# Kernel tuning notes

Hardware: AMD Instinct MI355X
Metric: run time of the kernel (lower is better)

## Reference

```python
import jax, jax.numpy as jnp
import numpy as np

N, F_IN, H1, H2, E = 100000, 256, 128, 64, 1600000


def _glorot(key, shape):
    lim = np.sqrt(6.0 / (shape[0] + shape[1]))
    return jax.random.uniform(key, shape, jnp.float32, -lim, lim)


def setup_inputs() -> dict:
    key = jax.random.key(0)
    ks = jax.random.split(key, 8)
    x = jax.random.normal(ks[0], (N, F_IN), jnp.float32)
    edge_index = jax.random.randint(ks[1], (2, E), 0, N, jnp.int64)
    return {
        "x": x,
        "w1": _glorot(ks[2], (F_IN, H1)),
        "b1": jnp.zeros((H1,), jnp.float32),
        "w2": _glorot(ks[3], (H1, H2)),
        "b2": jnp.zeros((H2,), jnp.float32),
        "w3": _glorot(ks[4], (H1, H2)),
        "b3": jnp.zeros((H2,), jnp.float32),
        "edge_index": edge_index,
    }


def _gcn_conv(x, w, b, src, dst, dinv_sqrt):
    # GCNConv: transform first, then symmetric-normalized aggregation with self-loops.
    h = x @ w                                   # [N, out]
    coef = dinv_sqrt[src] * dinv_sqrt[dst]      # [E]
    agg = jnp.zeros_like(h).at[dst].add(h[src] * coef[:, None])
    # self-loop contribution: coefficient deg^-1 per node
    agg = agg + h * (dinv_sqrt * dinv_sqrt)[:, None]
    return agg + b


def reference(x, w1, b1, w2, b2, w3, b3, edge_index):
    src, dst = edge_index[0], edge_index[1]
    n = x.shape[0]
    # degree including self-loop (edge weights all 1)
    deg = jnp.ones((n,), x.dtype).at[dst].add(1.0)
    dinv_sqrt = jax.lax.rsqrt(deg)
    hidden = jax.nn.relu(_gcn_conv(x, w1, b1, src, dst, dinv_sqrt))
    mu = _gcn_conv(hidden, w2, b2, src, dst, dinv_sqrt)
    logvar = _gcn_conv(hidden, w3, b3, src, dst, dinv_sqrt)
    return (mu, logvar)
```

## Files before the change

### kernel.cpp

```cpp
#include <hip/hip_runtime.h>


#define TPB 256
#define GSHIFT 9
#define GSIZE 512
#define PART_M 4096
#define GCAP 12288

typedef __attribute__((ext_vector_type(8))) short short8;
typedef __attribute__((ext_vector_type(4))) short short4v;
typedef __attribute__((ext_vector_type(4))) float floatx4;
typedef __attribute__((ext_vector_type(4))) unsigned int uint4v;

__device__ __forceinline__ void split2(float v, short& hi, short& lo) {
    unsigned u = __float_as_uint(v);
    float hf = __uint_as_float(u & 0xFFFF0000u);
    float lf = v - hf;
    hi = (short)(u >> 16);
    lo = (short)(__float_as_uint(lf) >> 16);
}

__device__ __forceinline__ short bf16_rtn(float v) {
    unsigned u = __float_as_uint(v);
    u += 0x7FFF + ((u >> 16) & 1);
    return (short)(u >> 16);
}

__device__ __forceinline__ void addrow(float* a, uint4v v) {
    a[0] += __uint_as_float(v[0] << 16); a[1] += __uint_as_float(v[0] & 0xFFFF0000u);
    a[2] += __uint_as_float(v[1] << 16); a[3] += __uint_as_float(v[1] & 0xFFFF0000u);
    a[4] += __uint_as_float(v[2] << 16); a[5] += __uint_as_float(v[2] & 0xFFFF0000u);
    a[6] += __uint_as_float(v[3] << 16); a[7] += __uint_as_float(v[3] & 0xFFFF0000u);
}

__device__ __forceinline__ void gather_accum(float* acc, const int* __restrict__ csr,
                                             int start, int deg, const uint4v* hp,
                                             int l16) {
    for (int jj = 0; jj < deg; jj += 16) {
        int rem = deg - jj;
        if (rem > 16) rem = 16;
        int il = (l16 < rem) ? l16 : rem - 1;
        int myIdx = csr[start + jj + il];
        int r = 0;
        for (; r + 3 < rem; r += 4) {
            int i0 = __shfl(myIdx, r + 0, 16);
            int i1 = __shfl(myIdx, r + 1, 16);
            int i2 = __shfl(myIdx, r + 2, 16);
            int i3 = __shfl(myIdx, r + 3, 16);
            uint4v v0 = hp[(size_t)i0 * 16 + l16];
            uint4v v1 = hp[(size_t)i1 * 16 + l16];
            uint4v v2 = hp[(size_t)i2 * 16 + l16];
            uint4v v3 = hp[(size_t)i3 * 16 + l16];
            addrow(acc, v0);
            addrow(acc, v1);
            addrow(acc, v2);
            addrow(acc, v3);
        }
        for (; r < rem; ++r) {
            int i = __shfl(myIdx, r, 16);
            addrow(acc, hp[(size_t)i * 16 + l16]);
        }
    }
}

__device__ __forceinline__ void gload_lds16(const void* g, void* l) {
    __builtin_amdgcn_global_load_lds(
        (const __attribute__((address_space(1))) unsigned int*)g,
        (__attribute__((address_space(3))) unsigned int*)l, 16, 0, 0);
}

__global__ __launch_bounds__(TPB) void prep_all(const float* __restrict__ w1,
                                                const float* __restrict__ w2,
                                                const float* __restrict__ b2,
                                                const float* __restrict__ w3,
                                                const float* __restrict__ b3,
                                                short* __restrict__ w1t_h,
                                                short* __restrict__ w1t_l,
                                                short* __restrict__ wct_h,
                                                short* __restrict__ wct_l,
                                                float* __restrict__ bcat,
                                                int* __restrict__ gcur) {
    int b = blockIdx.x, t0 = threadIdx.x;
    if (b < 128) {
        int t = b * TPB + t0;
        int k = t & 255, n = t >> 8;
        float v = w1[(size_t)k * 128 + n];
        short h, l;
        split2(v, h, l);
        w1t_h[t] = h;
        w1t_l[t] = l;
    } else if (b < 192) {
        int t = (b - 128) * TPB + t0;
        int k = t & 127, n = t >> 7;
        float v = (n < 64) ? w2[(size_t)k * 64 + n] : w3[(size_t)k * 64 + (n - 64)];
        short h, l;
        split2(v, h, l);
        wct_h[t] = h;
        wct_l[t] = l;
        if (t < 64) { bcat[t] = b2[t]; bcat[64 + t] = b3[t]; }
    } else {
        gcur[t0] = 0;
    }
}

__global__ __launch_bounds__(256) void partition_kernel(const int* __restrict__ src,
                                                        const int* __restrict__ dst,
                                                        int* __restrict__ gcur,
                                                        int* __restrict__ staged, int E) {
    __shared__ int sc[256];
    __shared__ int cur[256];
    __shared__ int gb[256];
    int t = threadIdx.x;
    int base = blockIdx.x * PART_M;
    int mloc = min(PART_M, E - base);
    int m4 = mloc >> 2;

    sc[t] = 0;
    cur[t] = 0;
    __syncthreads();
    const int4* d4 = (const int4*)(dst + base);
    const int4* s4 = (const int4*)(src + base);
    for (int k = t; k < m4; k += 256) {
        int4 v = d4[k];
        atomicAdd(&sc[v.x >> GSHIFT], 1);
        atomicAdd(&sc[v.y >> GSHIFT], 1);
        atomicAdd(&sc[v.z >> GSHIFT], 1);
        atomicAdd(&sc[v.w >> GSHIFT], 1);
    }
    for (int k = (m4 << 2) + t; k < mloc; k += 256)
        atomicAdd(&sc[dst[base + k] >> GSHIFT], 1);
    __syncthreads();
    int v = sc[t];
    gb[t] = v ? t * GCAP + atomicAdd(&gcur[t], v) : 0;
    __syncthreads();
    for (int k = t; k < m4; k += 256) {
        int4 dv = d4[k];
        int4 sv = s4[k];
        int b0 = dv.x >> GSHIFT;
        staged[gb[b0] + atomicAdd(&cur[b0], 1)] = (sv.x << GSHIFT) | (dv.x & (GSIZE - 1));
        int b1 = dv.y >> GSHIFT;
        staged[gb[b1] + atomicAdd(&cur[b1], 1)] = (sv.y << GSHIFT) | (dv.y & (GSIZE - 1));
        int b2 = dv.z >> GSHIFT;
        staged[gb[b2] + atomicAdd(&cur[b2], 1)] = (sv.z << GSHIFT) | (dv.z & (GSIZE - 1));
        int b3 = dv.w >> GSHIFT;
        staged[gb[b3] + atomicAdd(&cur[b3], 1)] = (sv.w << GSHIFT) | (dv.w & (GSIZE - 1));
    }
    for (int k = (m4 << 2) + t; k < mloc; k += 256) {
        int d = dst[base + k];
        int s = src[base + k];
        int b = d >> GSHIFT;
        staged[gb[b] + atomicAdd(&cur[b], 1)] = (s << GSHIFT) | (d & (GSIZE - 1));
    }
}

__global__ __launch_bounds__(512) void build_csr(const int* __restrict__ staged,
                                                 const int* __restrict__ gcur,
                                                 int* __restrict__ cnt,
                                                 float* __restrict__ dinv,
                                                 int* __restrict__ rowptr,
                                                 int* __restrict__ csr, int N) {
    __shared__ int pre[256];
    __shared__ int hist[512];
    __shared__ int sc[512];
    __shared__ int lrow[512];
    __shared__ int cur[512];
    int t = threadIdx.x;
    int g = blockIdx.x;
    int ngrp = (N + GSIZE - 1) >> GSHIFT;
    if (t < 256) pre[t] = (t < ngrp) ? gcur[t] : 0;
    hist[t] = 0;
    cur[t] = 0;
    __syncthreads();
#pragma unroll
    for (int off = 1; off < 256; off <<= 1) {
        int x = (t < 256 && t >= off) ? pre[t - off] : 0;
        __syncthreads();
        if (t < 256) pre[t] += x;
        __syncthreads();
    }
    int count = gcur[g];
    int s0_out = pre[g] - count;
    int s0_in = g * GCAP;
    for (int k = t; k < count; k += 512)
        atomicAdd(&hist[staged[s0_in + k] & (GSIZE - 1)], 1);
    __syncthreads();
    int v = hist[t];
    sc[t] = v;
    __syncthreads();
#pragma unroll
    for (int off = 1; off < 512; off <<= 1) {
        int x = (t >= off) ? sc[t - off] : 0;
        __syncthreads();
        sc[t] += x;
        __syncthreads();
    }
    int rp = s0_out + sc[t] - v;
    lrow[t] = rp;
    int node = (g << GSHIFT) + t;
    if (node < N) {
        rowptr[node] = rp;
        cnt[node] = v;
        dinv[node] = rsqrtf(1.0f + (float)v);
    }
    __syncthreads();
    for (int k = t; k < count; k += 512) {
        int p = staged[s0_in + k];
        int dl = p & (GSIZE - 1);
        int pos = lrow[dl] + atomicAdd(&cur[dl], 1);
        csr[pos] = p >> GSHIFT;
    }
}

__global__ __launch_bounds__(TPB) void gemm_mfma_f32in(const float* __restrict__ A,
                                                       const short* __restrict__ Bth,
                                                       const short* __restrict__ Btl,
                                                       const float* __restrict__ rs,
                                                       short* __restrict__ Cb, int M, int K) {
    __shared__ float Af[2][128 * 32];
    __shared__ short Bh[2][128 * 32];
    __shared__ short Bl[2][128 * 32];
    int t = threadIdx.x;
    int wave = t >> 6, lane = t & 63, quad = lane >> 4, l16 = lane & 15;
    int bm0 = blockIdx.x * 128;

    floatx4 acc[2][8];
#pragma unroll
    for (int mt = 0; mt < 2; ++mt)
#pragma unroll
        for (int nt = 0; nt < 8; ++nt) acc[mt][nt] = (floatx4){0.f, 0.f, 0.f, 0.f};

    auto stage = [&](int pb, int k0) {
#pragma unroll
        for (int i = 0; i < 4; ++i) {
            int g = i * 256 + t;
            int row = g >> 3, col = g & 7;
            int gr = bm0 + row;
            if (gr >= M) gr = M - 1;
            int scol = col ^ (row & 7);
            gload_lds16(A + (size_t)gr * K + k0 + scol * 4,
                        &Af[pb][(i * 256 + wave * 64) * 4]);
        }
#pragma unroll
        for (int i = 0; i < 2; ++i) {
            int g = i * 256 + t;
            int row = g >> 2, col = g & 3;
            int scol = col ^ ((row >> 1) & 3);
            size_t off = (size_t)row * K + k0 + scol * 8;
            int lb = (i * 256 + wave * 64) * 8;
            gload_lds16(Bth + off, &Bh[pb][lb]);
            gload_lds16(Btl + off, &Bl[pb][lb]);
        }
    };

    int nk = K >> 5;
    stage(0, 0);
    __syncthreads();
    int r0 = wave * 32 + l16;
    int ac0 = ((quad * 2 + 0) ^ (r0 & 7)) * 4;
    int ac1 = ((quad * 2 + 1) ^ (r0 & 7)) * 4;
    int bc = (quad ^ ((l16 >> 1) & 3)) * 8;
    for (int ks = 0; ks < nk; ++ks) {
        int pb = ks & 1;
        if (ks + 1 < nk) stage(pb ^ 1, (ks + 1) << 5);
        short8 a_h[2], a_l[2];
#pragma unroll
        for (int mt = 0; mt < 2; ++mt) {
            int r = r0 + mt * 16;
            float4 fa0 = *(const float4*)&Af[pb][r * 32 + ac0];
            float4 fa1 = *(const float4*)&Af[pb][r * 32 + ac1];
            short h, l;
            split2(fa0.x, h, l); a_h[mt][0] = h; a_l[mt][0] = l;
            split2(fa0.y, h, l); a_h[mt][1] = h; a_l[mt][1] = l;
            split2(fa0.z, h, l); a_h[mt][2] = h; a_l[mt][2] = l;
            split2(fa0.w, h, l); a_h[mt][3] = h; a_l[mt][3] = l;
            split2(fa1.x, h, l); a_h[mt][4] = h; a_l[mt][4] = l;
            split2(fa1.y, h, l); a_h[mt][5] = h; a_l[mt][5] = l;
            split2(fa1.z, h, l); a_h[mt][6] = h; a_l[mt][6] = l;
            split2(fa1.w, h, l); a_h[mt][7] = h; a_l[mt][7] = l;
        }
#pragma unroll
        for (int nt = 0; nt < 8; ++nt) {
            int bn = nt * 16 + l16;
            short8 b_h = *(const short8*)&Bh[pb][bn * 32 + bc];
            short8 b_l = *(const short8*)&Bl[pb][bn * 32 + bc];
#pragma unroll
            for (int mt = 0; mt < 2; ++mt) {
                acc[mt][nt] = __builtin_amdgcn_mfma_f32_16x16x32_bf16(a_l[mt], b_h, acc[mt][nt], 0, 0, 0);
                acc[mt][nt] = __builtin_amdgcn_mfma_f32_16x16x32_bf16(a_h[mt], b_l, acc[mt][nt], 0, 0, 0);
                acc[mt][nt] = __builtin_amdgcn_mfma_f32_16x16x32_bf16(a_h[mt], b_h, acc[mt][nt], 0, 0, 0);
            }
        }
        __syncthreads();
    }
#pragma unroll
    for (int mt = 0; mt < 2; ++mt)
#pragma unroll
        for (int reg = 0; reg < 4; ++reg) {
            int gr = bm0 + wave * 32 + mt * 16 + quad * 4 + reg;
            if (gr < M) {
                float s = rs[gr];
                short* cp = Cb + (size_t)gr * 128;
#pragma unroll
                for (int nt = 0; nt < 8; ++nt) cp[nt * 16 + l16] = bf16_rtn(acc[mt][nt][reg] * s);
            }
        }
}

__global__ __launch_bounds__(TPB) void gemm_mfma_bfin(const short* __restrict__ AH,
                                                      const short* __restrict__ AL,
                                                      const short* __restrict__ Bth,
                                                      const short* __restrict__ Btl,
                                                      const float* __restrict__ rs,
                                                      short* __restrict__ Cb, int M, int K) {
    __shared__ short Ah[2][128 * 32], Al[2][128 * 32];
    __shared__ short Bh[2][128 * 32], Bl[2][128 * 32];
    int t = threadIdx.x;
    int wave = t >> 6, lane = t & 63, quad = lane >> 4, l16 = lane & 15;
    int bm0 = blockIdx.x * 128;

    floatx4 acc[2][8];
#pragma unroll
    for (int mt = 0; mt < 2; ++mt)
#pragma unroll
        for (int nt = 0; nt < 8; ++nt) acc[mt][nt] = (floatx4){0.f, 0.f, 0.f, 0.f};

    auto stage = [&](int pb, int k0) {
#pragma unroll
        for (int i = 0; i < 2; ++i) {
            int g = i * 256 + t;
            int row = g >> 2, col = g & 3;
            int gr = bm0 + row;
            if (gr >= M) gr = M - 1;
            int scol = col ^ ((row >> 1) & 3);
            size_t off = (size_t)gr * K + k0 + scol * 8;
            int lb = (i * 256 + wave * 64) * 8;
            gload_lds16(AH + off, &Ah[pb][lb]);
            gload_lds16(AL + off, &Al[pb][lb]);
        }
#pragma unroll
        for (int i = 0; i < 2; ++i) {
            int g = i * 256 + t;
            int row = g >> 2, col = g & 3;
            int scol = col ^ ((row >> 1) & 3);
            size_t off = (size_t)row * K + k0 + scol * 8;
            int lb = (i * 256 + wave * 64) * 8;
            gload_lds16(Bth + off, &Bh[pb][lb]);
            gload_lds16(Btl + off, &Bl[pb][lb]);
        }
    };

    int nk = K >> 5;
    stage(0, 0);
    __syncthreads();
    int r0 = wave * 32 + l16;
    int ac = (quad ^ ((r0 >> 1) & 3)) * 8;
    int bc = (quad ^ ((l16 >> 1) & 3)) * 8;
    for (int ks = 0; ks < nk; ++ks) {
        int pb = ks & 1;
        if (ks + 1 < nk) stage(pb ^ 1, (ks + 1) << 5);
        short8 a_h[2], a_l[2];
#pragma unroll
        for (int mt = 0; mt < 2; ++mt) {
            int r = r0 + mt * 16;
            a_h[mt] = *(const short8*)&Ah[pb][r * 32 + ac];
            a_l[mt] = *(const short8*)&Al[pb][r * 32 + ac];
        }
#pragma unroll
        for (int nt = 0; nt < 8; ++nt) {
            int bn = nt * 16 + l16;
            short8 b_h = *(const short8*)&Bh[pb][bn * 32 + bc];
            short8 b_l = *(const short8*)&Bl[pb][bn * 32 + bc];
#pragma unroll
            for (int mt = 0; mt < 2; ++mt) {
                acc[mt][nt] = __builtin_amdgcn_mfma_f32_16x16x32_bf16(a_l[mt], b_h, acc[mt][nt], 0, 0, 0);
                acc[mt][nt] = __builtin_amdgcn_mfma_f32_16x16x32_bf16(a_h[mt], b_l, acc[mt][nt], 0, 0, 0);
                acc[mt][nt] = __builtin_amdgcn_mfma_f32_16x16x32_bf16(a_h[mt], b_h, acc[mt][nt], 0, 0, 0);
            }
        }
        __syncthreads();
    }
#pragma unroll
    for (int mt = 0; mt < 2; ++mt)
#pragma unroll
        for (int reg = 0; reg < 4; ++reg) {
            int gr = bm0 + wave * 32 + mt * 16 + quad * 4 + reg;
            if (gr < M) {
                float s = rs[gr];
                short* cp = Cb + (size_t)gr * 128;
#pragma unroll
                for (int nt = 0; nt < 8; ++nt) cp[nt * 16 + l16] = bf16_rtn(acc[mt][nt][reg] * s);
            }
        }
}

__global__ __launch_bounds__(TPB) void gather_hidden(const int* __restrict__ csr,
                                                     const int* __restrict__ rowptr,
                                                     const int* __restrict__ cnt,
                                                     const float* __restrict__ dinv,
                                                     const short* __restrict__ hs,
                                                     const float* __restrict__ b1,
                                                     short* __restrict__ hidH,
                                                     short* __restrict__ hidL, int N) {
    size_t t = (size_t)blockIdx.x * TPB + threadIdx.x;
    int nid = (int)(t >> 4);
    int lane = threadIdx.x & 15;
    if (nid >= N) return;
    int start = rowptr[nid];
    int deg = cnt[nid];
    const uint4v* hp = (const uint4v*)hs;
    float acc[8] = {0, 0, 0, 0, 0, 0, 0, 0};
    addrow(acc, hp[(size_t)nid * 16 + lane]);
    gather_accum(acc, csr, start, deg, hp, lane);
    float di = dinv[nid];
    float4 b0 = ((const float4*)b1)[lane * 2];
    float4 b1v = ((const float4*)b1)[lane * 2 + 1];
    float bb[8] = {b0.x, b0.y, b0.z, b0.w, b1v.x, b1v.y, b1v.z, b1v.w};
    unsigned hiw[8];
    short low[8];
#pragma unroll
    for (int i = 0; i < 8; ++i) {
        float h = fmaxf(fmaf(di, acc[i], bb[i]), 0.f);
        unsigned u = __float_as_uint(h);
        hiw[i] = u >> 16;
        float hf = __uint_as_float(u & 0xFFFF0000u);
        low[i] = bf16_rtn(h - hf);
    }
    uint4v ph, pl;
    ph[0] = hiw[0] | (hiw[1] << 16);
    ph[1] = hiw[2] | (hiw[3] << 16);
    ph[2] = hiw[4] | (hiw[5] << 16);
    ph[3] = hiw[6] | (hiw[7] << 16);
    pl[0] = (unsigned short)low[0] | ((unsigned)(unsigned short)low[1] << 16);
    pl[1] = (unsigned short)low[2] | ((unsigned)(unsigned short)low[3] << 16);
    pl[2] = (unsigned short)low[4] | ((unsigned)(unsigned short)low[5] << 16);
    pl[3] = (unsigned short)low[6] | ((unsigned)(unsigned short)low[7] << 16);
    ((uint4v*)hidH)[(size_t)nid * 16 + lane] = ph;
    ((uint4v*)hidL)[(size_t)nid * 16 + lane] = pl;
}

__global__ __launch_bounds__(TPB) void gather_out(const int* __restrict__ csr,
                                                  const int* __restrict__ rowptr,
                                                  const int* __restrict__ cnt,
                                                  const float* __restrict__ dinv,
                                                  const short* __restrict__ hs,
                                                  const float* __restrict__ bcat,
                                                  float* __restrict__ out, int N) {
    size_t t = (size_t)blockIdx.x * TPB + threadIdx.x;
    int nid = (int)(t >> 4);
    int lane = threadIdx.x & 15;
    if (nid >= N) return;
    int start = rowptr[nid];
    int deg = cnt[nid];
    const uint4v* hp = (const uint4v*)hs;
    float acc[8] = {0, 0, 0, 0, 0, 0, 0, 0};
    addrow(acc, hp[(size_t)nid * 16 + lane]);
    gather_accum(acc, csr, start, deg, hp, lane);
    float di = dinv[nid];
    float4 b0 = ((const float4*)bcat)[lane * 2];
    float4 b1v = ((const float4*)bcat)[lane * 2 + 1];
    floatx4 r0, r1;
    r0[0] = fmaf(di, acc[0], b0.x);
    r0[1] = fmaf(di, acc[1], b0.y);
    r0[2] = fmaf(di, acc[2], b0.z);
    r0[3] = fmaf(di, acc[3], b0.w);
    r1[0] = fmaf(di, acc[4], b1v.x);
    r1[1] = fmaf(di, acc[5], b1v.y);
    r1[2] = fmaf(di, acc[6], b1v.z);
    r1[3] = fmaf(di, acc[7], b1v.w);
    int f = lane * 8;
    float* dp = (f < 64) ? (out + (size_t)nid * 64 + f)
                         : (out + (size_t)N * 64 + (size_t)nid * 64 + (f - 64));
    __builtin_nontemporal_store(r0, (floatx4*)dp);
    __builtin_nontemporal_store(r1, (floatx4*)(dp + 4));
}

extern "C" void kernel_launch(void* const* d_in, const int* in_sizes, int n_in,
                              void* d_out, int out_size, void* d_ws, size_t ws_size,
                              hipStream_t stream) {
    const float* x  = (const float*)d_in[0];
    const float* w1 = (const float*)d_in[1];
    const float* b1 = (const float*)d_in[2];
    const float* w2 = (const float*)d_in[3];
    const float* b2 = (const float*)d_in[4];
    const float* w3 = (const float*)d_in[5];
    const float* b3 = (const float*)d_in[6];
    const int*   ei = (const int*)d_in[7];

    const int N = in_sizes[0] / 256;
    const int E = in_sizes[7] / 2;
    const int K1 = 256;

    float* out = (float*)d_out;

    size_t nh = (size_t)N * 128;
    short* hs1    = (short*)d_ws;
    short* hidH   = hs1 + nh;
    short* hidL   = hidH + nh;
    short* hs2    = hidL + nh;
    int*   cnt    = (int*)(hs2 + nh);
    float* dinv   = (float*)(cnt + N);
    int*   rowptr = (int*)(dinv + N);
    int*   cursor = rowptr + N;
    int*   bsum   = cursor + N;
    float* bcat   = (float*)(bsum + 512);
    short* w1t_h  = (short*)(bcat + 128);
    short* w1t_l  = w1t_h + 128 * 256;
    short* wct_h  = w1t_l + 128 * 256;
    short* wct_l  = wct_h + 128 * 128;
    int*   csr    = (int*)(wct_l + 128 * 128);

    const int* srcp = ei;
    const int* dstp = ei + E;

    const int ngrp = (N + GSIZE - 1) >> GSHIFT;
    int* gcur   = cursor;
    int* staged = (int*)hs2;

    prep_all<<<193, TPB, 0, stream>>>(w1, w2, b2, w3, b3, w1t_h, w1t_l, wct_h, wct_l,
                                      bcat, gcur);

    partition_kernel<<<(E + PART_M - 1) / PART_M, 256, 0, stream>>>(srcp, dstp, gcur,
                                                                    staged, E);
    build_csr<<<ngrp, 512, 0, stream>>>(staged, gcur, cnt, dinv, rowptr, csr, N);

    gemm_mfma_f32in<<<(N + 127) / 128, TPB, 0, stream>>>(x, w1t_h, w1t_l, dinv, hs1, N, K1);

    size_t gthreads = (size_t)N * 16;
    gather_hidden<<<(unsigned)((gthreads + TPB - 1) / TPB), TPB, 0, stream>>>(
        csr, rowptr, cnt, dinv, hs1, b1, hidH, hidL, N);

    gemm_mfma_bfin<<<(N + 127) / 128, TPB, 0, stream>>>(hidH, hidL, wct_h, wct_l, dinv, hs2, N, 128);

    gather_out<<<(unsigned)((gthreads + TPB - 1) / TPB), TPB, 0, stream>>>(
        csr, rowptr, cnt, dinv, hs2, bcat, out, N);
}
```

Baseline: 380.7 us.

## Fuse prep with partition and CSR build with first GEMM

Merges weight prep and edge partitioning into one launch, and runs the CSR build blocks and the first GEMM tiles in a single grid. The first GEMM no longer depends on dinv, so the source-side normalization moves into gather_hidden, which loads dinv per neighbor and applies it with an FMA. This removes two kernel launches and lets the CSR construction overlap the x@W1 GEMM. In exchange, gather_hidden does an extra dinv load and shuffle per edge, and gcur is now zeroed with a memset.

Result: no change. 374.5 us (-1.6%).

```diff
diff --git a/kernel.cpp b/kernel.cpp
--- a/kernel.cpp
+++ b/kernel.cpp
@@ -6,6 +6,7 @@
 #define GSIZE 512
 #define PART_M 4096
 #define GCAP 12288
+#define NPREP 192
 
 typedef __attribute__((ext_vector_type(8))) short short8;
 typedef __attribute__((ext_vector_type(4))) short short4v;
@@ -31,6 +32,17 @@
     a[2] += __uint_as_float(v[1] << 16); a[3] += __uint_as_float(v[1] & 0xFFFF0000u);
     a[4] += __uint_as_float(v[2] << 16); a[5] += __uint_as_float(v[2] & 0xFFFF0000u);
     a[6] += __uint_as_float(v[3] << 16); a[7] += __uint_as_float(v[3] & 0xFFFF0000u);
+}
+
+__device__ __forceinline__ void addrow_s(float* a, uint4v v, float s) {
+    a[0] = fmaf(s, __uint_as_float(v[0] << 16), a[0]);
+    a[1] = fmaf(s, __uint_as_float(v[0] & 0xFFFF0000u), a[1]);
+    a[2] = fmaf(s, __uint_as_float(v[1] << 16), a[2]);
+    a[3] = fmaf(s, __uint_as_float(v[1] & 0xFFFF0000u), a[3]);
+    a[4] = fmaf(s, __uint_as_float(v[2] << 16), a[4]);
+    a[5] = fmaf(s, __uint_as_float(v[2] & 0xFFFF0000u), a[5]);
+    a[6] = fmaf(s, __uint_as_float(v[3] << 16), a[6]);
+    a[7] = fmaf(s, __uint_as_float(v[3] & 0xFFFF0000u), a[7]);
 }
 
 __device__ __forceinline__ void gather_accum(float* acc, const int* __restrict__ csr,
@@ -63,58 +75,90 @@
     }
 }
 
+__device__ __forceinline__ void gather_accum_s(float* acc, const int* __restrict__ csr,
+                                               const float* __restrict__ dinv,
+                                               int start, int deg, const uint4v* hp,
+                                               int l16) {
+    for (int jj = 0; jj < deg; jj += 16) {
+        int rem = deg - jj;
+        if (rem > 16) rem = 16;
+        int il = (l16 < rem) ? l16 : rem - 1;
+        int myIdx = csr[start + jj + il];
+        float myD = dinv[myIdx];
+        int r = 0;
+        for (; r + 3 < rem; r += 4) {
+            int i0 = __shfl(myIdx, r + 0, 16);
+            int i1 = __shfl(myIdx, r + 1, 16);
+            int i2 = __shfl(myIdx, r + 2, 16);
+            int i3 = __shfl(myIdx, r + 3, 16);
+            float d0 = __shfl(myD, r + 0, 16);
+            float d1 = __shfl(myD, r + 1, 16);
+            float d2 = __shfl(myD, r + 2, 16);
+            float d3 = __shfl(myD, r + 3, 16);
+            uint4v v0 = hp[(size_t)i0 * 16 + l16];
+            uint4v v1 = hp[(size_t)i1 * 16 + l16];
+            uint4v v2 = hp[(size_t)i2 * 16 + l16];
+            uint4v v3 = hp[(size_t)i3 * 16 + l16];
+            addrow_s(acc, v0, d0);
+            addrow_s(acc, v1, d1);
+            addrow_s(acc, v2, d2);
+            addrow_s(acc, v3, d3);
+        }
+        for (; r < rem; ++r) {
+            int i = __shfl(myIdx, r, 16);
+            float d = __shfl(myD, r, 16);
+            addrow_s(acc, hp[(size_t)i * 16 + l16], d);
+        }
+    }
+}
+
 __device__ __forceinline__ void gload_lds16(const void* g, void* l) {
     __builtin_amdgcn_global_load_lds(
         (const __attribute__((address_space(1))) unsigned int*)g,
         (__attribute__((address_space(3))) unsigned int*)l, 16, 0, 0);
 }
 
-__global__ __launch_bounds__(TPB) void prep_all(const float* __restrict__ w1,
-                                                const float* __restrict__ w2,
-                                                const float* __restrict__ b2,
-                                                const float* __restrict__ w3,
-                                                const float* __restrict__ b3,
-                                                short* __restrict__ w1t_h,
-                                                short* __restrict__ w1t_l,
-                                                short* __restrict__ wct_h,
-                                                short* __restrict__ wct_l,
-                                                float* __restrict__ bcat,
-                                                int* __restrict__ gcur) {
-    int b = blockIdx.x, t0 = threadIdx.x;
+__global__ __launch_bounds__(TPB) void prep_part(const float* __restrict__ w1,
+                                                 const float* __restrict__ w2,
+                                                 const float* __restrict__ b2,
+                                                 const float* __restrict__ w3,
+                                                 const float* __restrict__ b3,
+                                                 short* __restrict__ w1t_h,
+                                                 short* __restrict__ w1t_l,
+                                                 short* __restrict__ wct_h,
+                                                 short* __restrict__ wct_l,
+                                                 float* __restrict__ bcat,
+                                                 const int* __restrict__ src,
+                                                 const int* __restrict__ dst,
+                                                 int* __restrict__ gcur,
+                                                 int* __restrict__ staged, int E) {
+    __shared__ int sc[256];
+    __shared__ int cur[256];
+    __shared__ int gb[256];
+    int b = blockIdx.x, t = threadIdx.x;
     if (b < 128) {
-        int t = b * TPB + t0;
-        int k = t & 255, n = t >> 8;
+        int i = b * TPB + t;
+        int k = i & 255, n = i >> 8;
         float v = w1[(size_t)k * 128 + n];
         short h, l;
         split2(v, h, l);
-        w1t_h[t] = h;
-        w1t_l[t] = l;
-    } else if (b < 192) {
-        int t = (b - 128) * TPB + t0;
-        int k = t & 127, n = t >> 7;
+        w1t_h[i] = h;
+        w1t_l[i] = l;
+        return;
+    } else if (b < NPREP) {
+        int i = (b - 128) * TPB + t;
+        int k = i & 127, n = i >> 7;
         float v = (n < 64) ? w2[(size_t)k * 64 + n] : w3[(size_t)k * 64 + (n - 64)];
         short h, l;
         split2(v, h, l);
-        wct_h[t] = h;
-        wct_l[t] = l;
-        if (t < 64) { bcat[t] = b2[t]; bcat[64 + t] = b3[t]; }
-    } else {
-        gcur[t0] = 0;
-    }
-}
-
-__global__ __launch_bounds__(256) void partition_kernel(const int* __restrict__ src,
-                                                        const int* __restrict__ dst,
-                                                        int* __restrict__ gcur,
-                                                        int* __restrict__ staged, int E) {
-    __shared__ int sc[256];
-    __shared__ int cur[256];
-    __shared__ int gb[256];
-    int t = threadIdx.x;
-    int base = blockIdx.x * PART_M;
+        wct_h[i] = h;
+        wct_l[i] = l;
+        if (i < 64) { bcat[i] = b2[i]; bcat[64 + i] = b3[i]; }
+        return;
+    }
+    int base = (b - NPREP) * PART_M;
     int mloc = min(PART_M, E - base);
     int m4 = mloc >> 2;
-
     sc[t] = 0;
     cur[t] = 0;
     __syncthreads();
@@ -140,88 +184,102 @@
         staged[gb[b0] + atomicAdd(&cur[b0], 1)] = (sv.x << GSHIFT) | (dv.x & (GSIZE - 1));
         int b1 = dv.y >> GSHIFT;
         staged[gb[b1] + atomicAdd(&cur[b1], 1)] = (sv.y << GSHIFT) | (dv.y & (GSIZE - 1));
-        int b2 = dv.z >> GSHIFT;
-        staged[gb[b2] + atomicAdd(&cur[b2], 1)] = (sv.z << GSHIFT) | (dv.z & (GSIZE - 1));
-        int b3 = dv.w >> GSHIFT;
-        staged[gb[b3] + atomicAdd(&cur[b3], 1)] = (sv.w << GSHIFT) | (dv.w & (GSIZE - 1));
+        int b2_ = dv.z >> GSHIFT;
+        staged[gb[b2_] + atomicAdd(&cur[b2_], 1)] = (sv.z << GSHIFT) | (dv.z & (GSIZE - 1));
+        int b3_ = dv.w >> GSHIFT;
+        staged[gb[b3_] + atomicAdd(&cur[b3_], 1)] = (sv.w << GSHIFT) | (dv.w & (GSIZE - 1));
     }
     for (int k = (m4 << 2) + t; k < mloc; k += 256) {
         int d = dst[base + k];
         int s = src[base + k];
-        int b = d >> GSHIFT;
-        staged[gb[b] + atomicAdd(&cur[b], 1)] = (s << GSHIFT) | (d & (GSIZE - 1));
-    }
-}
-
-__global__ __launch_bounds__(512) void build_csr(const int* __restrict__ staged,
+        int bb = d >> GSHIFT;
+        staged[gb[bb] + atomicAdd(&cur[bb], 1)] = (s << GSHIFT) | (d & (GSIZE - 1));
+    }
+}
+
+__global__ __launch_bounds__(TPB) void csr_gemm1(const int* __restrict__ staged,
                                                  const int* __restrict__ gcur,
                                                  int* __restrict__ cnt,
                                                  float* __restrict__ dinv,
                                                  int* __restrict__ rowptr,
-                                                 int* __restrict__ csr, int N) {
+                                                 int* __restrict__ csr,
+                                                 const float* __restrict__ A,
+                                                 const short* __restrict__ Bth,
+                                                 const short* __restrict__ Btl,
+                                                 short* __restrict__ Cb,
+                                                 int N, int K, int ngrp) {
     __shared__ int pre[256];
     __shared__ int hist[512];
-    __shared__ int sc[512];
+    __shared__ int psum[256];
     __shared__ int lrow[512];
-    __shared__ int cur[512];
-    int t = threadIdx.x;
-    int g = blockIdx.x;
-    int ngrp = (N + GSIZE - 1) >> GSHIFT;
-    if (t < 256) pre[t] = (t < ngrp) ? gcur[t] : 0;
-    hist[t] = 0;
-    cur[t] = 0;
-    __syncthreads();
-#pragma unroll
-    for (int off = 1; off < 256; off <<= 1) {
-        int x = (t < 256 && t >= off) ? pre[t - off] : 0;
-        __syncthreads();
-        if (t < 256) pre[t] += x;
-        __syncthreads();
-    }
-    int count = gcur[g];
-    int s0_out = pre[g] - count;
-    int s0_in = g * GCAP;
-    for (int k = t; k < count; k += 512)
-        atomicAdd(&hist[staged[s0_in + k] & (GSIZE - 1)], 1);
-    __syncthreads();
-    int v = hist[t];
-    sc[t] = v;
-    __syncthreads();
-#pragma unroll
-    for (int off = 1; off < 512; off <<= 1) {
-        int x = (t >= off) ? sc[t - off] : 0;
-        __syncthreads();
-        sc[t] += x;
-        __syncthreads();
-    }
-    int rp = s0_out + sc[t] - v;
-    lrow[t] = rp;
-    int node = (g << GSHIFT) + t;
-    if (node < N) {
-        rowptr[node] = rp;
-        cnt[node] = v;
-        dinv[node] = rsqrtf(1.0f + (float)v);
-    }
-    __syncthreads();
-    for (int k = t; k < count; k += 512) {
-        int p = staged[s0_in + k];
-        int dl = p & (GSIZE - 1);
-        int pos = lrow[dl] + atomicAdd(&cur[dl], 1);
-        csr[pos] = p >> GSHIFT;
-    }
-}
-
-__global__ __launch_bounds__(TPB) void gemm_mfma_f32in(const float* __restrict__ A,
-                                                       const short* __restrict__ Bth,
-                                                       const short* __restrict__ Btl,
-                                                       const float* __restrict__ rs,
-                                                       short* __restrict__ Cb, int M, int K) {
+    __shared__ int curq[512];
     __shared__ float Af[2][128 * 32];
     __shared__ short Bh[2][128 * 32];
     __shared__ short Bl[2][128 * 32];
     int t = threadIdx.x;
+
+    if ((int)blockIdx.x < ngrp) {
+        int g = blockIdx.x;
+        pre[t] = (t < ngrp) ? gcur[t] : 0;
+        hist[t] = 0;
+        hist[t + 256] = 0;
+        curq[t] = 0;
+        curq[t + 256] = 0;
+        __syncthreads();
+#pragma unroll
+        for (int off = 1; off < 256; off <<= 1) {
+            int x = (t >= off) ? pre[t - off] : 0;
+            __syncthreads();
+            pre[t] += x;
+            __syncthreads();
+        }
+        int count = gcur[g];
+        int s0_out = pre[g] - count;
+        int s0_in = g * GCAP;
+        for (int k = t; k < count; k += 256)
+            atomicAdd(&hist[staged[s0_in + k] & (GSIZE - 1)], 1);
+        __syncthreads();
+        int h0 = hist[2 * t], h1 = hist[2 * t + 1];
+        int ps = h0 + h1;
+        psum[t] = ps;
+        __syncthreads();
+#pragma unroll
+        for (int off = 1; off < 256; off <<= 1) {
+            int x = (t >= off) ? psum[t - off] : 0;
+            __syncthreads();
+            psum[t] += x;
+            __syncthreads();
+        }
+        int excl = psum[t] - ps;
+        int rp0 = s0_out + excl;
+        int rp1 = rp0 + h0;
+        lrow[2 * t] = rp0;
+        lrow[2 * t + 1] = rp1;
+        int node0 = (g << GSHIFT) + 2 * t;
+        int node1 = node0 + 1;
+        if (node0 < N) {
+            rowptr[node0] = rp0;
+            cnt[node0] = h0;
+            dinv[node0] = rsqrtf(1.0f + (float)h0);
+        }
+        if (node1 < N) {
+            rowptr[node1] = rp1;
+            cnt[node1] = h1;
+            dinv[node1] = rsqrtf(1.0f + (float)h1);
+        }
+        __syncthreads();
+        for (int k = t; k < count; k += 256) {
+            int p = staged[s0_in + k];
+            int dl = p & (GSIZE - 1);
+            int pos = lrow[dl] + atomicAdd(&curq[dl], 1);
+            csr[pos] = p >> GSHIFT;
+        }
+        return;
+    }
+
     int wave = t >> 6, lane = t & 63, quad = lane >> 4, l16 = lane & 15;
-    int bm0 = blockIdx.x * 128;
+    int bm0 = ((int)blockIdx.x - ngrp) * 128;
+    int M = N;
 
     floatx4 acc[2][8];
 #pragma unroll
@@ -298,10 +356,9 @@
         for (int reg = 0; reg < 4; ++reg) {
             int gr = bm0 + wave * 32 + mt * 16 + quad * 4 + reg;
             if (gr < M) {
-                float s = rs[gr];
                 short* cp = Cb + (size_t)gr * 128;
 #pragma unroll
-                for (int nt = 0; nt < 8; ++nt) cp[nt * 16 + l16] = bf16_rtn(acc[mt][nt][reg] * s);
+                for (int nt = 0; nt < 8; ++nt) cp[nt * 16 + l16] = bf16_rtn(acc[mt][nt][reg]);
             }
         }
 }
@@ -407,11 +464,11 @@
     if (nid >= N) return;
     int start = rowptr[nid];
     int deg = cnt[nid];
+    float di = dinv[nid];
     const uint4v* hp = (const uint4v*)hs;
     float acc[8] = {0, 0, 0, 0, 0, 0, 0, 0};
-    addrow(acc, hp[(size_t)nid * 16 + lane]);
-    gather_accum(acc, csr, start, deg, hp, lane);
-    float di = dinv[nid];
+    addrow_s(acc, hp[(size_t)nid * 16 + lane], di);
+    gather_accum_s(acc, csr, dinv, start, deg, hp, lane);
     float4 b0 = ((const float4*)b1)[lane * 2];
     float4 b1v = ((const float4*)b1)[lane * 2 + 1];
     float bb[8] = {b0.x, b0.y, b0.z, b0.w, b1v.x, b1v.y, b1v.z, b1v.w};
@@ -516,14 +573,16 @@
     int* gcur   = cursor;
     int* staged = (int*)hs2;
 
-    prep_all<<<193, TPB, 0, stream>>>(w1, w2, b2, w3, b3, w1t_h, w1t_l, wct_h, wct_l,
-                                      bcat, gcur);
-
-    partition_kernel<<<(E + PART_M - 1) / PART_M, 256, 0, stream>>>(srcp, dstp, gcur,
-                                                                    staged, E);
-    build_csr<<<ngrp, 512, 0, stream>>>(staged, gcur, cnt, dinv, rowptr, csr, N);
-
-    gemm_mfma_f32in<<<(N + 127) / 128, TPB, 0, stream>>>(x, w1t_h, w1t_l, dinv, hs1, N, K1);
+    hipMemsetAsync(gcur, 0, 256 * sizeof(int), stream);
+
+    int nPart = (E + PART_M - 1) / PART_M;
+    prep_part<<<NPREP + nPart, TPB, 0, stream>>>(w1, w2, b2, w3, b3, w1t_h, w1t_l,
+                                                 wct_h, wct_l, bcat, srcp, dstp, gcur,
+                                                 staged, E);
+
+    int gtiles = (N + 127) / 128;
+    csr_gemm1<<<ngrp + gtiles, TPB, 0, stream>>>(staged, gcur, cnt, dinv, rowptr, csr,
+                                                 x, w1t_h, w1t_l, hs1, N, K1, ngrp);
 
     size_t gthreads = (size_t)N * 16;
     gather_hidden<<<(unsigned)((gthreads + TPB - 1) / TPB), TPB, 0, stream>>>(
```
